# Optimization experiments

Measured on AMD Instinct MI355X. Metric: run time of the kernel, lower is better.

## Reference

```python
import jax, jax.numpy as jnp
import numpy as np

B, N = 4, 8192
D = 128
DEPTH = 4
LEAF = 32
HEADS = 4
HD = D // HEADS
SLOTS = 24
RANKS = [20, 32, 52, 82]                      # rank at encoder step j (fine -> coarse)
EXP = [RANKS[j] * (2 ** j) for j in range(DEPTH)]  # HODLR head output dims


def _rope_tables(seq_len, dim):
    inv_freq = 1.0 / (10000.0 ** (jnp.arange(0, dim, 2, dtype=jnp.float32) / dim))
    t = jnp.arange(seq_len, dtype=jnp.float32)
    freqs = t[:, None] * inv_freq[None, :]
    emb = jnp.concatenate([freqs, freqs], axis=-1)   # [S, dim]
    return jnp.cos(emb), jnp.sin(emb)


def _rotate_half(x):
    x1, x2 = jnp.split(x, 2, axis=-1)
    return jnp.concatenate([-x2, x1], axis=-1)


def _layernorm(x, g, b, eps=1e-5):
    mu = jnp.mean(x, -1, keepdims=True)
    var = jnp.mean((x - mu) ** 2, -1, keepdims=True)
    return (x - mu) * jax.lax.rsqrt(var + eps) * g + b


def _block_attn(h, qkv_w, qkv_b, pw, pb, cos, sin):
    Bc, Nc, C = h.shape
    nb = Nc // LEAF
    xb = h.reshape(Bc * nb, LEAF, C)
    qkv = (xb @ qkv_w + qkv_b).reshape(Bc * nb, LEAF, 3, HEADS, HD)
    qkv = qkv.transpose(2, 0, 3, 1, 4)               # [3, BN, H, L, hd]
    q, k, v = qkv[0], qkv[1], qkv[2]
    q = q * cos + _rotate_half(q) * sin              # full-dim RoPE (rope_dim == head_dim)
    k = k * cos + _rotate_half(k) * sin
    attn = jax.nn.softmax(jnp.einsum('bhqd,bhkd->bhqk', q, k) * (HD ** -0.5), axis=-1)
    o = jnp.einsum('bhqk,bhkd->bhqd', attn, v).transpose(0, 2, 1, 3).reshape(Bc * nb, LEAF, C)
    return (o @ pw + pb).reshape(Bc, Nc, C)


def _forward(x, cen_w, cen_b, nbr_w, nbr_b, inp_w, inp_b,
             leafp_w, leafp_b, leafh_w, leafh_b, log_scale_leaf,
             ln1_g, ln1_b, qkv_w, qkv_b, attnp_w, attnp_b,
             ln2_g, ln2_b, mlp1_w, mlp1_b, mlp2_w, mlp2_b, ds_w, ds_b,
             hu_w0, hu_b0, hv_w0, hv_b0, hu_w1, hu_b1, hv_w1, hv_b1,
             hu_w2, hu_b2, hv_w2, hv_b2, hu_w3, hu_b3, hv_w3, hv_b3):
    Bx, Nx, _ = x.shape
    # --- SymmetricNeighborEmbed (24 neighbor slots, vectorized) ---
    pos_i = x[..., 0:3]
    diag_i = x[..., 3:4]
    h_center = jnp.concatenate([pos_i, diag_i], -1) @ cen_w + cen_b          # [B,N,D]
    nb_feat = x[..., 4:4 + 5 * SLOTS].reshape(Bx, Nx, SLOTS, 5)
    rel = nb_feat[..., 0:1]
    pos_j = nb_feat[..., 1:4]
    w_ij = nb_feat[..., 4:5]
    active = (w_ij != 0.0).astype(x.dtype)
    feat = jnp.concatenate([rel * active, (pos_j - pos_i[:, :, None, :]) * active, w_ij], -1)
    e = (feat @ nbr_w + nbr_b) * active                                       # [B,N,24,D]
    h = h_center + jnp.sum(e, axis=2)
    h = h @ inp_w + inp_b
    # --- leaf dense diagonal blocks ---
    nl = Nx // LEAF
    hl = h.reshape(Bx, nl, LEAF, D) @ leafp_w + leafp_b                       # [B,nl,32,32]
    u_leaf = hl @ leafh_w + leafh_b
    dense = jnp.einsum('blik,bljk->blij', u_leaf, u_leaf) * jnp.exp(log_scale_leaf)
    diag_a = x[..., 3]                                                        # scale_A defaults to 1.0
    mask = jnp.abs(diag_a) > 1e-6
    new_diag = jnp.where(mask, 1.0 / jnp.where(mask, diag_a, 1.0), 1.0).reshape(Bx, nl, LEAF)
    dense = dense + new_diag[..., :, None] * jnp.eye(LEAF, dtype=x.dtype)
    # --- down-only encoder: transformer block -> HODLR head -> 2:1 downsample ---
    cos, sin = _rope_tables(LEAF, HD)
    hu = [(hu_w0, hu_b0), (hu_w1, hu_b1), (hu_w2, hu_b2), (hu_w3, hu_b3)]
    hv = [(hv_w0, hv_b0), (hv_w1, hv_b1), (hv_w2, hv_b2), (hv_w3, hv_b3)]
    us, vs = [], []
    for j in range(DEPTH):
        a = _block_attn(_layernorm(h, ln1_g[j], ln1_b[j]),
                        qkv_w[j], qkv_b[j], attnp_w[j], attnp_b[j], cos, sin)
        h = h + a
        m = _layernorm(h, ln2_g[j], ln2_b[j])
        m = jax.nn.gelu(m @ mlp1_w[j] + mlp1_b[j], approximate=False) @ mlp2_w[j] + mlp2_b[j]
        h = h + m
        us.append((h @ hu[j][0] + hu[j][1]).reshape(Bx, Nx, RANKS[j]))
        vs.append((h @ hv[j][0] + hv[j][1]).reshape(Bx, Nx, RANKS[j]))
        Bh, n, c = h.shape
        h = h.reshape(Bh, n // 2, 2 * c) @ ds_w[j] + ds_b[j]
    # single flat output: dense leaf blocks + all U/V HODLR factors
    return jnp.concatenate([dense.reshape(Bx, -1),
                            jnp.concatenate(us, -1).reshape(Bx, -1),
                            jnp.concatenate(vs, -1).reshape(Bx, -1)], -1)


def setup_inputs():
    key = jax.random.key(0)
    ks = iter(jax.random.split(key, 64))
    def rn(shape, s=0.05):
        return jax.random.normal(next(ks), shape, jnp.float32) * s
    z = lambda *s: jnp.zeros(s, jnp.float32)
    o = lambda *s: jnp.ones(s, jnp.float32)
    inp = {
        'x': jax.random.normal(next(ks), (B, N, 4 + 5 * SLOTS), jnp.float32),
        'cen_w': rn((4, D)), 'cen_b': z(D),
        'nbr_w': rn((5, D)), 'nbr_b': z(D),
        'inp_w': rn((D, D)), 'inp_b': z(D),
        'leafp_w': rn((D, LEAF)), 'leafp_b': z(LEAF),
        'leafh_w': rn((LEAF, LEAF), 0.01), 'leafh_b': z(LEAF),
        'log_scale_leaf': jnp.full((1,), np.log(0.01), jnp.float32),
        'ln1_g': o(DEPTH, D), 'ln1_b': z(DEPTH, D),
        'qkv_w': rn((DEPTH, D, 3 * D)), 'qkv_b': z(DEPTH, 3 * D),
        'attnp_w': rn((DEPTH, D, D)), 'attnp_b': z(DEPTH, D),
        'ln2_g': o(DEPTH, D), 'ln2_b': z(DEPTH, D),
        'mlp1_w': rn((DEPTH, D, 4 * D)), 'mlp1_b': z(DEPTH, 4 * D),
        'mlp2_w': rn((DEPTH, 4 * D, D)), 'mlp2_b': z(DEPTH, D),
        'ds_w': rn((DEPTH, 2 * D, D)), 'ds_b': z(DEPTH, D),
    }
    for j in range(DEPTH):
        inp['hu_w%d' % j] = rn((D, EXP[j]), 0.01)
        inp['hu_b%d' % j] = z(EXP[j])
        inp['hv_w%d' % j] = rn((D, EXP[j]), 0.01)
        inp['hv_b%d' % j] = z(EXP[j])
    return inp


def reference(x, cen_w, cen_b, nbr_w, nbr_b, inp_w, inp_b,
              leafp_w, leafp_b, leafh_w, leafh_b, log_scale_leaf,
              ln1_g, ln1_b, qkv_w, qkv_b, attnp_w, attnp_b,
              ln2_g, ln2_b, mlp1_w, mlp1_b, mlp2_w, mlp2_b, ds_w, ds_b,
              hu_w0, hu_b0, hv_w0, hv_b0, hu_w1, hu_b1, hv_w1, hv_b1,
              hu_w2, hu_b2, hv_w2, hv_b2, hu_w3, hu_b3, hv_w3, hv_b3):
    return _forward(x, cen_w, cen_b, nbr_w, nbr_b, inp_w, inp_b,
                    leafp_w, leafp_b, leafh_w, leafh_b, log_scale_leaf,
                    ln1_g, ln1_b, qkv_w, qkv_b, attnp_w, attnp_b,
                    ln2_g, ln2_b, mlp1_w, mlp1_b, mlp2_w, mlp2_b, ds_w, ds_b,
                    hu_w0, hu_b0, hv_w0, hv_b0, hu_w1, hu_b1, hv_w1, hv_b1,
                    hu_w2, hu_b2, hv_w2, hv_b2, hu_w3, hu_b3, hv_w3, hv_b3)
```

## Files before the change

kernel.cpp:

```cpp
#include <hip/hip_runtime.h>
#include <math.h>

#define DEV __device__ __forceinline__

constexpr int XFv = 124;
constexpr size_t OPB   = 3309568;
constexpr size_t UBASE = 262144;
constexpr size_t VBASE = 1785856;
constexpr int UVWID = 186;

using bfrag  = __attribute__((ext_vector_type(8))) short;
using f32x4v = __attribute__((ext_vector_type(4))) float;

DEV float* at4p(float* base, int t, int c0, int W) {
  return base + t * W + ((c0 + 4 * t) & (W - 1));
}
DEV float& at1r(float* base, int t, int c, int W) {
  return base[t * W + (((c & ~3) + 4 * t) & (W - 1)) + (c & 3)];
}
DEV float4 ld4g(const float* p) { return *(const float4*)p; }
DEV void fma4(float4& a, float s, const float4& w) {
  a.x += s * w.x; a.y += s * w.y; a.z += s * w.z; a.w += s * w.w;
}
DEV float gelu_fast(float x) {
  float x2 = x * x;
  float z = x * (1.5957691216057308f + 0.0713551f * x2);
  float e = __expf(z);
  float r = 1.0f - __frcp_rn(e + 1.0f);
  return x * r;
}
DEV ushort f2bf(float x) {
  unsigned u = __float_as_uint(x);
  unsigned r = (u + 0x7fffu + ((u >> 16) & 1u)) >> 16;
  return (ushort)r;
}
DEV void stb128(ushort* b, int row, int col, float v) {
  b[row * 128 + (((col & ~7) + 8 * row) & 127) + (col & 7)] = f2bf(v);
}

__global__ __launch_bounds__(256) void wprep_all_kernel(
    const float* __restrict__ src0, ushort* __restrict__ dst0, int K, int N) {
  size_t off = (size_t)blockIdx.z * K * N;
  const float* src = src0 + off;
  ushort* dst = dst0 + off;
  __shared__ float S[64][65];
  int tid = threadIdx.x;
  int k0 = blockIdx.x * 64, n0 = blockIdx.y * 64;
  for (int i = tid; i < 64 * 64; i += 256) {
    int kk = i >> 6, nn = i & 63;
    S[kk][nn] = src[(size_t)(k0 + kk) * N + n0 + nn];
  }
  __syncthreads();
  int n = tid >> 2, kq = tid & 3;
  unsigned pk[8];
#pragma unroll
  for (int i = 0; i < 8; i++) {
    int k = kq * 16 + 2 * i;
    pk[i] = (unsigned)f2bf(S[k][n]) | ((unsigned)f2bf(S[k + 1][n]) << 16);
  }
  unsigned* dp = (unsigned*)&dst[(size_t)(n0 + n) * K + k0 + kq * 16];
#pragma unroll
  for (int i = 0; i < 8; i++) dp[i] = pk[i];
}

struct UVDesc {
  const float* src[8];
  ushort* dst[8];
  int expj[8];
  int npad[8];
};
__global__ __launch_bounds__(256) void uvprep_all_kernel(UVDesc d) {
  int mi = blockIdx.y;
  int i = blockIdx.x * 256 + threadIdx.x;
  int expj = d.expj[mi];
  if (i >= d.npad[mi] * 128) return;
  int n = i >> 7, k = i & 127;
  d.dst[mi][(size_t)n * 128 + k] =
      (n < expj) ? f2bf(d.src[mi][(size_t)k * expj + n]) : (ushort)0;
}

__global__ __launch_bounds__(128) void weff_prep_kernel(
    const float* __restrict__ cw, const float* __restrict__ cb,
    const float* __restrict__ nw, const float* __restrict__ nb,
    const float* __restrict__ iw, const float* __restrict__ ib,
    float* __restrict__ weff, float* __restrict__ ropetab) {
  __shared__ float S[11 * 128];
  int tid = threadIdx.x;
  for (int i = tid; i < 512; i += 128) S[i] = cw[i];
  for (int i = tid; i < 640; i += 128) S[512 + i] = nw[i];
  S[1152 + tid] = nb[tid];
  S[1280 + tid] = cb[tid];
  __syncthreads();
  float acc[11];
#pragma unroll
  for (int r = 0; r < 10; r++) acc[r] = 0.f;
  acc[10] = ib[tid];
  for (int k = 0; k < 128; k++) {
    float w = iw[k * 128 + tid];
#pragma unroll
    for (int r = 0; r < 11; r++) acc[r] += S[r * 128 + k] * w;
  }
#pragma unroll
  for (int r = 0; r < 11; r++) weff[r * 128 + tid] = acc[r];
  for (int idx = tid; idx < 512; idx += 128) {
    int pos = idx >> 4, d = idx & 15;
    float ang = (float)pos * expf(-0.57564627324851148f * (float)d);
    ropetab[idx] = cosf(ang);
    ropetab[512 + idx] = sinf(ang);
  }
}

__global__ __launch_bounds__(256) void node_embed2_kernel(
    const float* __restrict__ x, const float* __restrict__ weff,
    float* __restrict__ h) {
  __shared__ float XR[64 * XFv];
  __shared__ float RF[64][11];
  __shared__ __align__(16) float WE[11 * 128];
  int tid = threadIdx.x;
  int node0 = blockIdx.x * 64;
  for (int i = tid; i < 64 * XFv; i += 256)
    XR[i] = x[(size_t)node0 * XFv + i];
  for (int i = tid; i < 11 * 128; i += 256) WE[i] = weff[i];
  __syncthreads();
  {
    int nn = tid >> 2, sl = tid & 3;
    const float* xr = XR + nn * XFv;
    float p0 = xr[0], p1 = xr[1], p2 = xr[2];
    float g[6] = {0.f, 0.f, 0.f, 0.f, 0.f, 0.f};
#pragma unroll
    for (int s = 0; s < 6; s++) {
      const float* f = xr + 4 + 5 * (sl * 6 + s);
      float w = f[4];
      if (w != 0.0f) {
        g[0] += f[0]; g[1] += f[1] - p0; g[2] += f[2] - p1;
        g[3] += f[3] - p2; g[4] += w; g[5] += 1.0f;
      }
    }
#pragma unroll
    for (int i = 0; i < 6; i++) {
      g[i] += __shfl_xor(g[i], 1);
      g[i] += __shfl_xor(g[i], 2);
    }
    if (sl == 0) {
      RF[nn][0] = p0; RF[nn][1] = p1; RF[nn][2] = p2; RF[nn][3] = xr[3];
#pragma unroll
      for (int i = 0; i < 6; i++) RF[nn][4 + i] = g[i];
    }
  }
  __syncthreads();
  {
    int w = tid >> 6, lane = tid & 63;
    int c4 = lane & 31, hi = lane >> 5;
    const float4* WE4 = (const float4*)WE;
#pragma unroll
    for (int rr = 0; rr < 8; rr++) {
      int node = w * 16 + rr * 2 + hi;
      float4 acc = WE4[10 * 32 + c4];
#pragma unroll
      for (int f = 0; f < 10; f++)
        fma4(acc, RF[node][f], WE4[f * 32 + c4]);
      *(float4*)&h[(size_t)(node0 + node) * 128 + c4 * 4] = acc;
    }
  }
}

__global__ __launch_bounds__(256) void leaf_dense_kernel(
    const float* __restrict__ h, const float* __restrict__ x,
    const float* __restrict__ lpw, const float* __restrict__ lpb,
    const float* __restrict__ lhw, const float* __restrict__ lhb,
    const float* __restrict__ lsc, float* __restrict__ out) {
  __shared__ __align__(16) float HS[32 * 128];
  __shared__ __align__(16) float HL[32 * 32];
  __shared__ __align__(16) float UL[32 * 32];
  int tid = threadIdx.x;
  int leaf = blockIdx.x;
  size_t base = (size_t)leaf * (32 * 128);
  for (int i = tid; i < 32 * 128; i += 256) {
    int t = i >> 7, c = i & 127;
    at1r(HS, t, c, 128) = h[base + i];
  }
  __syncthreads();
  int t = tid & 31, cg = tid >> 5;
  {
    float4 acc = ld4g(&lpb[4 * cg]);
    for (int k4 = 0; k4 < 128; k4 += 4) {
      float4 xv = *(const float4*)at4p(HS, t, k4, 128);
      float xa[4] = {xv.x, xv.y, xv.z, xv.w};
#pragma unroll
      for (int kk = 0; kk < 4; kk++)
        fma4(acc, xa[kk], ld4g(&lpw[(k4 + kk) * 32 + 4 * cg]));
    }
    *(float4*)at4p(HL, t, 4 * cg, 32) = acc;
  }
  __syncthreads();
  {
    float4 acc = ld4g(&lhb[4 * cg]);
    for (int k4 = 0; k4 < 32; k4 += 4) {
      float4 xv = *(const float4*)at4p(HL, t, k4, 32);
      float xa[4] = {xv.x, xv.y, xv.z, xv.w};
#pragma unroll
      for (int kk = 0; kk < 4; kk++)
        fma4(acc, xa[kk], ld4g(&lhw[(k4 + kk) * 32 + 4 * cg]));
    }
    *(float4*)at4p(UL, t, 4 * cg, 32) = acc;
  }
  __syncthreads();
  {
    float scale = expf(lsc[0]);
    float acc[4] = {0.f, 0.f, 0.f, 0.f};
    for (int k4 = 0; k4 < 32; k4 += 4) {
      float4 xv = *(const float4*)at4p(UL, t, k4, 32);
      float xa[4] = {xv.x, xv.y, xv.z, xv.w};
#pragma unroll
      for (int kk = 0; kk < 4; kk++) {
        int k = k4 + kk;
#pragma unroll
        for (int i2 = 0; i2 < 4; i2++)
          acc[i2] += xa[kk] * at1r(UL, 4 * cg + i2, k, 32);
      }
    }
    int b = leaf >> 8, l = leaf & 255;
#pragma unroll
    for (int i2 = 0; i2 < 4; i2++) {
      int c = 4 * cg + i2;
      float v = acc[i2] * scale;
      if (c == t) {
        float dg = x[(size_t)(leaf * 32 + t) * XFv + 3];
        v += (fabsf(dg) > 1e-6f) ? (1.0f / dg) : 1.0f;
      }
      out[(size_t)b * OPB + (size_t)l * 1024 + t * 32 + c] = v;
    }
  }
}

__global__ __launch_bounds__(256, 4) void layer_mfma_kernel(
    float* __restrict__ h,
    const float* __restrict__ lng, const float* __restrict__ lnb,
    const ushort* __restrict__ wqkvt, const float* __restrict__ bqkv,
    const ushort* __restrict__ wpt, const float* __restrict__ pb,
    const float* __restrict__ rt,
    const float* __restrict__ ln2g, const float* __restrict__ ln2b,
    const ushort* __restrict__ w1t, const float* __restrict__ b1,
    const ushort* __restrict__ w2t, const float* __restrict__ b2) {
  __shared__ __align__(16) ushort SM[20480];
  ushort* XN = SM;
  ushort* QB = SM + 4096;
  ushort* KB = SM + 8192;
  ushort* VT = SM + 12288;
  ushort* HC1 = SM + 16384;
  float*  HS = (float*)(SM + 8192);
  int tid = threadIdx.x;
  size_t base = (size_t)blockIdx.x * (32 * 128);
  int w = tid >> 6, l = tid & 63, lm = l & 15, q = l >> 4;

  {
    int m8 = tid >> 3, p8 = tid & 7;
    const float* row = h + base + m8 * 128 + p8 * 16;
    float v[16];
    float s = 0.f;
#pragma unroll
    for (int i = 0; i < 16; i += 4) {
      float4 t4 = ld4g(row + i);
      v[i] = t4.x; v[i + 1] = t4.y; v[i + 2] = t4.z; v[i + 3] = t4.w;
      s += t4.x + t4.y + t4.z + t4.w;
    }
    s += __shfl_xor(s, 1); s += __shfl_xor(s, 2); s += __shfl_xor(s, 4);
    float mu = s * (1.0f / 128.0f);
    float s2 = 0.f;
#pragma unroll
    for (int i = 0; i < 16; i++) { float d = v[i] - mu; s2 += d * d; }
    s2 += __shfl_xor(s2, 1); s2 += __shfl_xor(s2, 2); s2 += __shfl_xor(s2, 4);
    float rs = rsqrtf(s2 * (1.0f / 128.0f) + 1e-5f);
    unsigned* XW = (unsigned*)XN;
#pragma unroll
    for (int i = 0; i < 16; i += 2) {
      int c = p8 * 16 + i;
      float x0 = (v[i] - mu) * rs * lng[c] + lnb[c];
      float x1 = (v[i + 1] - mu) * rs * lng[c + 1] + lnb[c + 1];
      int kp = c >> 1;
      XW[m8 * 64 + ((kp + 4 * m8) & 63)] =
          (unsigned)f2bf(x0) | ((unsigned)f2bf(x1) << 16);
    }
  }
  __syncthreads();

  {
    f32x4v acc[2][6];
#pragma unroll
    for (int mt = 0; mt < 2; mt++)
#pragma unroll
      for (int nt = 0; nt < 6; nt++) acc[mt][nt] = (f32x4v){0.f, 0.f, 0.f, 0.f};
    for (int ks = 0; ks < 4; ks++) {
      bfrag a[2];
#pragma unroll
      for (int mt = 0; mt < 2; mt++) {
        int mm = mt * 16 + lm;
        a[mt] = *(const bfrag*)&XN[mm * 128 + ((ks * 32 + q * 8 + 8 * mm) & 127)];
      }
#pragma unroll
      for (int nt = 0; nt < 6; nt++) {
        int n = w * 96 + nt * 16 + lm;
        bfrag b = *(const bfrag*)&wqkvt[(size_t)n * 128 + ks * 32 + q * 8];
#pragma unroll
        for (int mt = 0; mt < 2; mt++)
          acc[mt][nt] = __builtin_amdgcn_mfma_f32_16x16x32_bf16(
              a[mt], b, acc[mt][nt], 0, 0, 0);
      }
    }
    float csA[4] = {}, snA[4] = {}, csB[4] = {}, snB[4] = {};
    if (w < 3) {
#pragma unroll
      for (int r = 0; r < 4; r++) {
        int pa = q * 4 + r;
        csA[r] = rt[pa * 16 + lm];        snA[r] = rt[512 + pa * 16 + lm];
        csB[r] = rt[(pa + 16) * 16 + lm]; snB[r] = rt[512 + (pa + 16) * 16 + lm];
      }
    }
#pragma unroll
    for (int p2 = 0; p2 < 3; p2++) {
      int g = w * 6 + 2 * p2;
      int ne = g * 16 + lm;
      if (g < 16) {
        float be = bqkv[ne], bo = bqkv[ne + 16];
        ushort* dst = (g < 8) ? QB : KB;
        int de = (g < 8) ? ne : ne - 128;
#pragma unroll
        for (int mt = 0; mt < 2; mt++)
#pragma unroll
          for (int r = 0; r < 4; r++) {
            int mm = mt * 16 + q * 4 + r;
            float cs = (mt & 1) ? csB[r] : csA[r];
            float sn = (mt & 1) ? snB[r] : snA[r];
            float e = acc[mt][2 * p2][r] + be;
            float o = acc[mt][2 * p2 + 1][r] + bo;
            stb128(dst, mm, de, e * cs - o * sn);
            stb128(dst, mm, de + 16, o * cs + e * sn);
          }
      } else {
#pragma unroll
        for (int h2 = 0; h2 < 2; h2++) {
          int nt = 2 * p2 + h2;
          int nv = (g + h2) * 16 + lm;
          int dv = nv - 256;
          float bv = bqkv[nv];
#pragma unroll
          for (int mt = 0; mt < 2; mt++) {
            int t0 = mt * 16 + q * 4;
            short4 pk;
            pk.x = (short)f2bf(acc[mt][nt][0] + bv);
            pk.y = (short)f2bf(acc[mt][nt][1] + bv);
            pk.z = (short)f2bf(acc[mt][nt][2] + bv);
            pk.w = (short)f2bf(acc[mt][nt][3] + bv);
            *(short4*)&VT[dv * 32 + (((t0 & ~7) + 8 * dv) & 31) + (t0 & 7)] = pk;
          }
        }
      }
    }
  }
  __syncthreads();

  ushort* SP = XN;
  {
    int head = w;
    f32x4v sc[2][2];
#pragma unroll
    for (int a2 = 0; a2 < 2; a2++)
#pragma unroll
      for (int b2 = 0; b2 < 2; b2++) sc[a2][b2] = (f32x4v){0.f, 0.f, 0.f, 0.f};
    bfrag qa[2], kb[2];
#pragma unroll
    for (int mt2 = 0; mt2 < 2; mt2++) {
      int row = mt2 * 16 + lm;
      qa[mt2] = *(const bfrag*)&QB[row * 128 + ((head * 32 + q * 8 + 8 * row) & 127)];
    }
#pragma unroll
    for (int nt2 = 0; nt2 < 2; nt2++) {
      int kt = nt2 * 16 + lm;
      kb[nt2] = *(const bfrag*)&KB[kt * 128 + ((head * 32 + q * 8 + 8 * kt) & 127)];
    }
#pragma unroll
    for (int mt2 = 0; mt2 < 2; mt2++)
#pragma unroll
      for (int nt2 = 0; nt2 < 2; nt2++)
        sc[mt2][nt2] = __builtin_amdgcn_mfma_f32_16x16x32_bf16(
            qa[mt2], kb[nt2], sc[mt2][nt2], 0, 0, 0);
    const float scl = 0.17677669529663688f;
#pragma unroll
    for (int mt2 = 0; mt2 < 2; mt2++)
#pragma unroll
      for (int nt2 = 0; nt2 < 2; nt2++)
#pragma unroll
        for (int r = 0; r < 4; r++) {
          int qt = mt2 * 16 + q * 4 + r;
          int kc = nt2 * 16 + lm;
          SP[head * 1024 + qt * 32 + (((kc & ~7) + 8 * qt) & 31) + (kc & 7)] =
              f2bf(sc[mt2][nt2][r] * scl);
        }
  }
  __syncthreads();

  {
    int rowid = tid >> 1, half = tid & 1;
    int head = rowid >> 5, qt = rowid & 31;
    ushort* rowp = SP + head * 1024 + qt * 32 + half * 16;
    float v[16];
#pragma unroll
    for (int pc = 0; pc < 2; pc++) {
      uint4 ch = *(const uint4*)&rowp[pc * 8];
      unsigned uu[4] = {ch.x, ch.y, ch.z, ch.w};
#pragma unroll
      for (int i2 = 0; i2 < 4; i2++) {
        v[pc * 8 + 2 * i2]     = __uint_as_float(uu[i2] << 16);
        v[pc * 8 + 2 * i2 + 1] = __uint_as_float(uu[i2] & 0xffff0000u);
      }
    }
    float mx = -1e30f;
#pragma unroll
    for (int i = 0; i < 16; i++) mx = fmaxf(mx, v[i]);
    mx = fmaxf(mx, __shfl_xor(mx, 1));
    float s = 0.f;
#pragma unroll
    for (int i = 0; i < 16; i++) { v[i] = __expf(v[i] - mx); s += v[i]; }
    s += __shfl_xor(s, 1);
    float inv = 1.0f / s;
#pragma unroll
    for (int pc = 0; pc < 2; pc++) {
      uint4 ch;
      unsigned uu[4];
#pragma unroll
      for (int i2 = 0; i2 < 4; i2++)
        uu[i2] = (unsigned)f2bf(v[pc * 8 + 2 * i2] * inv) |
                 ((unsigned)f2bf(v[pc * 8 + 2 * i2 + 1] * inv) << 16);
      ch.x = uu[0]; ch.y = uu[1]; ch.z = uu[2]; ch.w = uu[3];
      *(uint4*)&rowp[pc * 8] = ch;
    }
  }
  __syncthreads();

  ushort* OB = QB;
  {
    int head = w;
    f32x4v ov[2][2];
#pragma unroll
    for (int a2 = 0; a2 < 2; a2++)
#pragma unroll
      for (int b2 = 0; b2 < 2; b2++) ov[a2][b2] = (f32x4v){0.f, 0.f, 0.f, 0.f};
    bfrag pa[2], vb2[2];
#pragma unroll
    for (int mt2 = 0; mt2 < 2; mt2++) {
      int qt = mt2 * 16 + lm;
      pa[mt2] = *(const bfrag*)&SP[head * 1024 + qt * 32 + ((q * 8 + 8 * qt) & 31)];
    }
#pragma unroll
    for (int nt2 = 0; nt2 < 2; nt2++) {
      int gdim = head * 32 + nt2 * 16 + lm;
      vb2[nt2] = *(const bfrag*)&VT[gdim * 32 + ((q * 8 + 8 * gdim) & 31)];
    }
#pragma unroll
    for (int mt2 = 0; mt2 < 2; mt2++)
#pragma unroll
      for (int nt2 = 0; nt2 < 2; nt2++)
        ov[mt2][nt2] = __builtin_amdgcn_mfma_f32_16x16x32_bf16(
            pa[mt2], vb2[nt2], ov[mt2][nt2], 0, 0, 0);
#pragma unroll
    for (int mt2 = 0; mt2 < 2; mt2++)
#pragma unroll
      for (int nt2 = 0; nt2 < 2; nt2++)
#pragma unroll
        for (int r = 0; r < 4; r++) {
          int qt = mt2 * 16 + q * 4 + r;
          int gdim = head * 32 + nt2 * 16 + lm;
          stb128(OB, qt, gdim, ov[mt2][nt2][r]);
        }
  }
  __syncthreads();

  {
    f32x4v po[2][2];
#pragma unroll
    for (int mt = 0; mt < 2; mt++)
#pragma unroll
      for (int nt = 0; nt < 2; nt++) po[mt][nt] = (f32x4v){0.f, 0.f, 0.f, 0.f};
    for (int ks = 0; ks < 4; ks++) {
      bfrag a[2];
#pragma unroll
      for (int mt = 0; mt < 2; mt++) {
        int mm = mt * 16 + lm;
        a[mt] = *(const bfrag*)&OB[mm * 128 + ((ks * 32 + q * 8 + 8 * mm) & 127)];
      }
#pragma unroll
      for (int nt = 0; nt < 2; nt++) {
        int n = w * 32 + nt * 16 + lm;
        bfrag b = *(const bfrag*)&wpt[(size_t)n * 128 + ks * 32 + q * 8];
#pragma unroll
        for (int mt = 0; mt < 2; mt++)
          po[mt][nt] = __builtin_amdgcn_mfma_f32_16x16x32_bf16(
              a[mt], b, po[mt][nt], 0, 0, 0);
      }
    }
#pragma unroll
    for (int nt = 0; nt < 2; nt++) {
      int n = w * 32 + nt * 16 + lm;
      float bv = pb[n];
#pragma unroll
      for (int mt = 0; mt < 2; mt++)
#pragma unroll
        for (int r = 0; r < 4; r++) {
          int mm = mt * 16 + q * 4 + r;
          at1r(HS, mm, n, 128) = po[mt][nt][r] + bv;
        }
    }
  }
  __syncthreads();

  {
    int j = tid & 31;
    int c0 = j * 4;
    float g0 = ln2g[c0], g1 = ln2g[c0 + 1], g2 = ln2g[c0 + 2], g3 = ln2g[c0 + 3];
    float e0 = ln2b[c0], e1 = ln2b[c0 + 1], e2 = ln2b[c0 + 2], e3 = ln2b[c0 + 3];
    unsigned* XW = (unsigned*)XN;
#pragma unroll
    for (int k2 = 0; k2 < 4; k2++) {
      int idx = tid + 256 * k2;
      int tok = idx >> 5;
      float4 hg = ld4g(&h[base + (size_t)idx * 4]);
      float4 ao = *(const float4*)at4p(HS, tok, 4 * j, 128);
      float4 hn;
      hn.x = hg.x + ao.x; hn.y = hg.y + ao.y;
      hn.z = hg.z + ao.z; hn.w = hg.w + ao.w;
      *(float4*)at4p(HS, tok, 4 * j, 128) = hn;
      float s = hn.x + hn.y + hn.z + hn.w;
      s += __shfl_xor(s, 1); s += __shfl_xor(s, 2); s += __shfl_xor(s, 4);
      s += __shfl_xor(s, 8); s += __shfl_xor(s, 16);
      float mu = s * (1.0f / 128.0f);
      float d0 = hn.x - mu, d1 = hn.y - mu, d2 = hn.z - mu, d3 = hn.w - mu;
      float s2 = d0 * d0 + d1 * d1 + d2 * d2 + d3 * d3;
      s2 += __shfl_xor(s2, 1); s2 += __shfl_xor(s2, 2); s2 += __shfl_xor(s2, 4);
      s2 += __shfl_xor(s2, 8); s2 += __shfl_xor(s2, 16);
      float rs = rsqrtf(s2 * (1.0f / 128.0f) + 1e-5f);
      float x0 = d0 * rs * g0 + e0;
      float x1 = d1 * rs * g1 + e1;
      float x2 = d2 * rs * g2 + e2;
      float x3 = d3 * rs * g3 + e3;
      int kp = 2 * j;
      XW[tok * 64 + ((kp + 4 * tok) & 63)] =
          (unsigned)f2bf(x0) | ((unsigned)f2bf(x1) << 16);
      XW[tok * 64 + ((kp + 1 + 4 * tok) & 63)] =
          (unsigned)f2bf(x2) | ((unsigned)f2bf(x3) << 16);
    }
  }
  __syncthreads();

  ushort* HC0 = QB;
  f32x4v acc2[2][2];
#pragma unroll
  for (int mt = 0; mt < 2; mt++)
#pragma unroll
    for (int nt = 0; nt < 2; nt++) acc2[mt][nt] = (f32x4v){0.f, 0.f, 0.f, 0.f};

  auto mlp1_calc = [&](int hc, f32x4v A1[2][2]) {
#pragma unroll
    for (int mt = 0; mt < 2; mt++)
#pragma unroll
      for (int nt = 0; nt < 2; nt++) A1[mt][nt] = (f32x4v){0.f, 0.f, 0.f, 0.f};
#pragma unroll
    for (int ks = 0; ks < 4; ks++) {
      bfrag a[2];
#pragma unroll
      for (int mt = 0; mt < 2; mt++) {
        int mm = mt * 16 + lm;
        a[mt] = *(const bfrag*)&XN[mm * 128 + ((ks * 32 + q * 8 + 8 * mm) & 127)];
      }
#pragma unroll
      for (int nt = 0; nt < 2; nt++) {
        int n = hc * 128 + w * 32 + nt * 16 + lm;
        bfrag b = *(const bfrag*)&w1t[(size_t)n * 128 + ks * 32 + q * 8];
#pragma unroll
        for (int mt = 0; mt < 2; mt++)
          A1[mt][nt] = __builtin_amdgcn_mfma_f32_16x16x32_bf16(
              a[mt], b, A1[mt][nt], 0, 0, 0);
      }
    }
  };
  auto gelu_store = [&](int hc, f32x4v A1[2][2], ushort* HCd) {
#pragma unroll
    for (int nt = 0; nt < 2; nt++) {
      int nl = w * 32 + nt * 16 + lm;
      float b1v = b1[hc * 128 + nl];
#pragma unroll
      for (int mt = 0; mt < 2; mt++)
#pragma unroll
        for (int r = 0; r < 4; r++) {
          int mm = mt * 16 + q * 4 + r;
          float val = gelu_fast(A1[mt][nt][r] + b1v);
          HCd[mm * 128 + (((nl & ~7) + 8 * mm) & 127) + (nl & 7)] = f2bf(val);
        }
    }
  };
  auto mlp2_calc = [&](int hc, ushort* HCr) {
#pragma unroll
    for (int ks = 0; ks < 4; ks++) {
      bfrag a[2];
#pragma unroll
      for (int mt = 0; mt < 2; mt++) {
        int mm = mt * 16 + lm;
        a[mt] = *(const bfrag*)&HCr[mm * 128 + ((ks * 32 + q * 8 + 8 * mm) & 127)];
      }
#pragma unroll
      for (int nt = 0; nt < 2; nt++) {
        int n = w * 32 + nt * 16 + lm;
        bfrag b = *(const bfrag*)&w2t[(size_t)n * 512 + hc * 128 + ks * 32 + q * 8];
#pragma unroll
        for (int mt = 0; mt < 2; mt++)
          acc2[mt][nt] = __builtin_amdgcn_mfma_f32_16x16x32_bf16(
              a[mt], b, acc2[mt][nt], 0, 0, 0);
      }
    }
  };

  f32x4v a1A[2][2], a1B[2][2];
  mlp1_calc(0, a1A);
  gelu_store(0, a1A, HC0);
  __syncthreads();
  mlp1_calc(1, a1B);
  mlp2_calc(0, HC0);
  gelu_store(1, a1B, HC1);
  __syncthreads();
  mlp1_calc(2, a1A);
  mlp2_calc(1, HC1);
  gelu_store(2, a1A, HC0);
  __syncthreads();
  mlp1_calc(3, a1B);
  mlp2_calc(2, HC0);
  gelu_store(3, a1B, HC1);
  __syncthreads();
  mlp2_calc(3, HC1);

#pragma unroll
  for (int nt = 0; nt < 2; nt++) {
    int n = w * 32 + nt * 16 + lm;
    float b2v = b2[n];
#pragma unroll
    for (int mt = 0; mt < 2; mt++)
#pragma unroll
      for (int r = 0; r < 4; r++) {
        int mm = mt * 16 + q * 4 + r;
        h[base + (size_t)mm * 128 + n] = at1r(HS, mm, n, 128) + acc2[mt][nt][r] + b2v;
      }
  }
}

template <int EXPJ, int RANK, int LVL, int NSPLIT>
__global__ __launch_bounds__(256) void uvds_kernel(
    const float* __restrict__ h,
    const ushort* __restrict__ uwt, const float* __restrict__ ub,
    const ushort* __restrict__ vwt, const float* __restrict__ vb,
    float* __restrict__ ustg, float* __restrict__ vstg,
    float* __restrict__ hout,
    const ushort* __restrict__ dwt, const float* __restrict__ dsb) {
  constexpr int NT16 = (EXPJ + 15) / 16;
  constexpr int NJOBS = 2 * NT16;
  __shared__ __align__(16) ushort XN[64 * 128];
  int tid = threadIdx.x;
  int t0 = blockIdx.x * 64;
  size_t base = (size_t)t0 * 128;
  {
    int m = tid >> 2, p = tid & 3;
    const float* row = h + base + m * 128 + p * 32;
    unsigned* XW = (unsigned*)XN;
#pragma unroll
    for (int i = 0; i < 32; i += 4) {
      float4 t4 = ld4g(row + i);
      int kp = (p * 32 + i) >> 1;
      XW[m * 64 + ((kp + 4 * m) & 63)] =
          (unsigned)f2bf(t4.x) | ((unsigned)f2bf(t4.y) << 16);
      XW[m * 64 + ((kp + 1 + 4 * m) & 63)] =
          (unsigned)f2bf(t4.z) | ((unsigned)f2bf(t4.w) << 16);
    }
  }
  __syncthreads();
  int w = tid >> 6, l = tid & 63, lm = l & 15, q = l >> 4;
  int gw = w + 4 * blockIdx.y;
  for (int jj = gw; jj < NJOBS; jj += 4 * NSPLIT) {
    int uvsel = jj & 1, nt = jj >> 1;
    const ushort* wt = uvsel ? vwt : uwt;
    const float* bias = uvsel ? vb : ub;
    float* stg = uvsel ? vstg : ustg;
    f32x4v acc[4];
#pragma unroll
    for (int mt = 0; mt < 4; mt++) acc[mt] = (f32x4v){0.f, 0.f, 0.f, 0.f};
    for (int ks = 0; ks < 4; ks++) {
      bfrag b = *(const bfrag*)&wt[(size_t)(nt * 16 + lm) * 128 + ks * 32 + q * 8];
#pragma unroll
      for (int mt = 0; mt < 4; mt++) {
        int mm = mt * 16 + lm;
        int ke = ks * 32 + q * 8;
        bfrag a = *(const bfrag*)&XN[mm * 128 + ((ke + 8 * mm) & 127)];
        acc[mt] = __builtin_amdgcn_mfma_f32_16x16x32_bf16(a, b, acc[mt], 0, 0, 0);
      }
    }
    int c = nt * 16 + lm;
    if (c < EXPJ) {
      float bv = bias[c];
#pragma unroll
      for (int mt = 0; mt < 4; mt++)
#pragma unroll
        for (int r = 0; r < 4; r++) {
          int mm = mt * 16 + q * 4 + r;
          stg[(size_t)(t0 + mm) * EXPJ + c] = acc[mt][r] + bv;
        }
    }
  }
  if constexpr (LVL < 3) {
    if (blockIdx.y == 0) {
      f32x4v dacc[2][2];
#pragma unroll
      for (int mt = 0; mt < 2; mt++)
#pragma unroll
        for (int nt = 0; nt < 2; nt++) dacc[mt][nt] = (f32x4v){0.f, 0.f, 0.f, 0.f};
      for (int ks = 0; ks < 8; ks++) {
        bfrag a[2];
#pragma unroll
        for (int mt = 0; mt < 2; mt++) {
          int rr = mt * 16 + lm;
          int tok = 2 * rr + (ks >> 2);
          int c2 = (ks & 3) * 32 + q * 8;
          a[mt] = *(const bfrag*)&XN[tok * 128 + ((c2 + 8 * tok) & 127)];
        }
#pragma unroll
        for (int nt = 0; nt < 2; nt++) {
          int n = w * 32 + nt * 16 + lm;
          bfrag b = *(const bfrag*)&dwt[(size_t)n * 256 + ks * 32 + q * 8];
#pragma unroll
          for (int mt = 0; mt < 2; mt++)
            dacc[mt][nt] = __builtin_amdgcn_mfma_f32_16x16x32_bf16(
                a[mt], b, dacc[mt][nt], 0, 0, 0);
        }
      }
      size_t ob2 = (size_t)blockIdx.x * (32 * 128);
#pragma unroll
      for (int nt = 0; nt < 2; nt++) {
        int n = w * 32 + nt * 16 + lm;
        float bv = dsb[n];
#pragma unroll
        for (int mt = 0; mt < 2; mt++)
#pragma unroll
          for (int r = 0; r < 4; r++) {
            int mm = mt * 16 + q * 4 + r;
            hout[ob2 + (size_t)mm * 128 + n] = dacc[mt][nt][r] + bv;
          }
      }
    }
  }
}

struct StgPtrs { const float* u[4]; const float* v[4]; };
__global__ __launch_bounds__(256) void uv_assemble_kernel(
    StgPtrs sp, float* __restrict__ out) {
  __shared__ unsigned char JL[93];
  __shared__ unsigned char CM[93];
  int tid = threadIdx.x;
  if (tid < 93) {
    int c = 2 * tid;
    int j = (c < 20) ? 0 : (c < 52) ? 1 : (c < 104) ? 2 : 3;
    int coff = (j == 0) ? 0 : (j == 1) ? 20 : (j == 2) ? 52 : 104;
    JL[tid] = (unsigned char)j;
    CM[tid] = (unsigned char)(c - coff);
  }
  __syncthreads();
  int g0 = blockIdx.x * 32;
  for (int i = tid; i < 32 * 93; i += 256) {
    int rr = i / 93, cp = i - rr * 93;
    int g = g0 + rr;
    int b = g >> 13, n = g & 8191;
    int j = JL[cp], cm = CM[cp];
    int expj, rank;
    if (j == 0)      { expj = 20;  rank = 20; }
    else if (j == 1) { expj = 64;  rank = 32; }
    else if (j == 2) { expj = 208; rank = 52; }
    else             { expj = 656; rank = 82; }
    int tok = (b << (13 - j)) + (n >> j);
    int cdiv = n & ((1 << j) - 1);
    size_t si = (size_t)tok * expj + cdiv * rank + cm;
    size_t ob = (size_t)b * OPB + (size_t)n * UVWID + 2 * cp;
    *(float2*)&out[ob + UBASE] = *(const float2*)&sp.u[j][si];
    *(float2*)&out[ob + VBASE] = *(const float2*)&sp.v[j][si];
  }
}

extern "C" void kernel_launch(void* const* d_in, const int* in_sizes, int n_in,
                              void* d_out, int out_size, void* d_ws, size_t ws_size,
                              hipStream_t stream) {
  const float* x       = (const float*)d_in[0];
  const float* cen_w   = (const float*)d_in[1];
  const float* cen_b   = (const float*)d_in[2];
  const float* nbr_w   = (const float*)d_in[3];
  const float* nbr_b   = (const float*)d_in[4];
  const float* inp_w   = (const float*)d_in[5];
  const float* inp_b   = (const float*)d_in[6];
  const float* leafp_w = (const float*)d_in[7];
  const float* leafp_b = (const float*)d_in[8];
  const float* leafh_w = (const float*)d_in[9];
  const float* leafh_b = (const float*)d_in[10];
  const float* lscale  = (const float*)d_in[11];
  const float* ln1_g   = (const float*)d_in[12];
  const float* ln1_b   = (const float*)d_in[13];
  const float* qkv_w   = (const float*)d_in[14];
  const float* qkv_b   = (const float*)d_in[15];
  const float* attnp_w = (const float*)d_in[16];
  const float* attnp_b = (const float*)d_in[17];
  const float* ln2_g   = (const float*)d_in[18];
  const float* ln2_b   = (const float*)d_in[19];
  const float* mlp1_w  = (const float*)d_in[20];
  const float* mlp1_b  = (const float*)d_in[21];
  const float* mlp2_w  = (const float*)d_in[22];
  const float* mlp2_b  = (const float*)d_in[23];
  const float* ds_w    = (const float*)d_in[24];
  const float* ds_b    = (const float*)d_in[25];
  const float* huw[4], *hub[4], *hvw[4], *hvb[4];
  for (int j = 0; j < 4; j++) {
    huw[j] = (const float*)d_in[26 + 4 * j];
    hub[j] = (const float*)d_in[27 + 4 * j];
    hvw[j] = (const float*)d_in[28 + 4 * j];
    hvb[j] = (const float*)d_in[29 + 4 * j];
  }
  float* out = (float*)d_out;
  float* hA = (float*)d_ws;
  float* hB = hA + (size_t)4 * 8192 * 128;
  ushort* w1t = (ushort*)(hB + (size_t)2097152);
  ushort* w2t = w1t + (size_t)4 * 65536;
  ushort* uvt = w2t + (size_t)4 * 65536;
  const int NPAD[4] = {32, 64, 208, 656};
  ushort* uwt[4]; ushort* vwt[4];
  ushort* p = uvt;
  for (int j = 0; j < 4; j++) {
    uwt[j] = p; p += (size_t)NPAD[j] * 128;
    vwt[j] = p; p += (size_t)NPAD[j] * 128;
  }
  ushort* wqkvt = p;
  ushort* wpt   = wqkvt + (size_t)4 * 384 * 128;
  ushort* dswt  = wpt + (size_t)4 * 128 * 128;
  float* weff   = (float*)(dswt + (size_t)4 * 128 * 256);
  float* ropetab = weff + 1408;
  const size_t STG[4] = {32768ull * 20, 16384ull * 64, 8192ull * 208, 4096ull * 656};
  float* ustg[4]; float* vstg[4];
  float* sp2 = ropetab + 1024;
  for (int j = 0; j < 4; j++) {
    ustg[j] = sp2; sp2 += STG[j];
    vstg[j] = sp2; sp2 += STG[j];
  }
  const int EXPJ_[4] = {20, 64, 208, 656};

  weff_prep_kernel<<<1, 128, 0, stream>>>(
      cen_w, cen_b, nbr_w, nbr_b, inp_w, inp_b, weff, ropetab);
  wprep_all_kernel<<<dim3(2, 8, 4), 256, 0, stream>>>(mlp1_w, w1t, 128, 512);
  wprep_all_kernel<<<dim3(8, 2, 4), 256, 0, stream>>>(mlp2_w, w2t, 512, 128);
  wprep_all_kernel<<<dim3(2, 6, 4), 256, 0, stream>>>(qkv_w, wqkvt, 128, 384);
  wprep_all_kernel<<<dim3(2, 2, 4), 256, 0, stream>>>(attnp_w, wpt, 128, 128);
  wprep_all_kernel<<<dim3(4, 2, 4), 256, 0, stream>>>(ds_w, dswt, 256, 128);
  {
    UVDesc d;
    for (int j = 0; j < 4; j++) {
      d.src[2 * j] = huw[j];     d.dst[2 * j] = uwt[j];
      d.src[2 * j + 1] = hvw[j]; d.dst[2 * j + 1] = vwt[j];
      d.expj[2 * j] = EXPJ_[j];  d.expj[2 * j + 1] = EXPJ_[j];
      d.npad[2 * j] = NPAD[j];   d.npad[2 * j + 1] = NPAD[j];
    }
    uvprep_all_kernel<<<dim3(328, 8), 256, 0, stream>>>(d);
  }

  node_embed2_kernel<<<(4 * 8192) / 64, 256, 0, stream>>>(x, weff, hA);
  leaf_dense_kernel<<<(4 * 8192) / 32, 256, 0, stream>>>(
      hA, x, leafp_w, leafp_b, leafh_w, leafh_b, lscale, out);

  layer_mfma_kernel<<<32768 / 32, 256, 0, stream>>>(
      hA, ln1_g, ln1_b, wqkvt, qkv_b, wpt, attnp_b, ropetab,
      ln2_g, ln2_b, w1t, mlp1_b, w2t, mlp2_b);
  uvds_kernel<20, 20, 0, 1><<<dim3(512, 1), 256, 0, stream>>>(
      hA, uwt[0], hub[0], vwt[0], hvb[0], ustg[0], vstg[0],
      hB, dswt, ds_b);

  layer_mfma_kernel<<<16384 / 32, 256, 0, stream>>>(
      hB, ln1_g + 128, ln1_b + 128, wqkvt + 49152, qkv_b + 384,
      wpt + 16384, attnp_b + 128, ropetab,
      ln2_g + 128, ln2_b + 128, w1t + 65536, mlp1_b + 512,
      w2t + 65536, mlp2_b + 128);
  uvds_kernel<64, 32, 1, 2><<<dim3(256, 2), 256, 0, stream>>>(
      hB, uwt[1], hub[1], vwt[1], hvb[1], ustg[1], vstg[1],
      hA, dswt + 32768, ds_b + 128);

  layer_mfma_kernel<<<8192 / 32, 256, 0, stream>>>(
      hA, ln1_g + 256, ln1_b + 256, wqkvt + 98304, qkv_b + 768,
      wpt + 32768, attnp_b + 256, ropetab,
      ln2_g + 256, ln2_b + 256, w1t + 131072, mlp1_b + 1024,
      w2t + 131072, mlp2_b + 256);
  uvds_kernel<208, 52, 2, 4><<<dim3(128, 4), 256, 0, stream>>>(
      hA, uwt[2], hub[2], vwt[2], hvb[2], ustg[2], vstg[2],
      hB, dswt + 65536, ds_b + 256);

  layer_mfma_kernel<<<4096 / 32, 256, 0, stream>>>(
      hB, ln1_g + 384, ln1_b + 384, wqkvt + 147456, qkv_b + 1152,
      wpt + 49152, attnp_b + 384, ropetab,
      ln2_g + 384, ln2_b + 384, w1t + 196608, mlp1_b + 1536,
      w2t + 196608, mlp2_b + 384);
  uvds_kernel<656, 82, 3, 8><<<dim3(64, 8), 256, 0, stream>>>(
      hB, uwt[3], hub[3], vwt[3], hvb[3], ustg[3], vstg[3],
      hA , dswt , ds_b );

  {
    StgPtrs sp;
    for (int j = 0; j < 4; j++) { sp.u[j] = ustg[j]; sp.v[j] = vstg[j]; }
    uv_assemble_kernel<<<32768 / 32, 256, 0, stream>>>(sp, out);
  }
  (void)in_sizes; (void)n_in; (void)out_size; (void)ws_size;
}
```

Measured before the change: 419.7 us.

## Fuse HODLR U/V heads and downsample into transformer layer epilogue

For the first three levels, the layer kernel now keeps its final residual output in shared memory, converts it to bf16, and computes the U/V head projections and the 2:1 downsample GEMM directly in its epilogue. This removes the separate uvds launches and the global round trip of the layer output for those levels. The last level still uses the standalone uvds kernel without the downsample. The cost is that all U/V output tiles for a 32-token block are now handled by only four waves, which serializes more work per block and adds shared-memory pressure and syncs to the layer kernel.

```diff
diff --git a/kernel.cpp b/kernel.cpp
--- a/kernel.cpp
+++ b/kernel.cpp
@@ -233,6 +233,7 @@
   }
 }
 
+template <int EXPJ, int RANK, int LVL, bool FUSE>
 __global__ __launch_bounds__(256, 4) void layer_mfma_kernel(
     float* __restrict__ h,
     const float* __restrict__ lng, const float* __restrict__ lnb,
@@ -241,7 +242,12 @@
     const float* __restrict__ rt,
     const float* __restrict__ ln2g, const float* __restrict__ ln2b,
     const ushort* __restrict__ w1t, const float* __restrict__ b1,
-    const ushort* __restrict__ w2t, const float* __restrict__ b2) {
+    const ushort* __restrict__ w2t, const float* __restrict__ b2,
+    const ushort* __restrict__ uwt, const float* __restrict__ ub,
+    const ushort* __restrict__ vwt, const float* __restrict__ vb,
+    float* __restrict__ ustg, float* __restrict__ vstg,
+    float* __restrict__ hout,
+    const ushort* __restrict__ dwt, const float* __restrict__ dsb) {
   __shared__ __align__(16) ushort SM[20480];
   ushort* XN = SM;
   ushort* QB = SM + 4096;
@@ -636,17 +642,114 @@
   __syncthreads();
   mlp2_calc(3, HC1);
 
-#pragma unroll
-  for (int nt = 0; nt < 2; nt++) {
-    int n = w * 32 + nt * 16 + lm;
-    float b2v = b2[n];
-#pragma unroll
-    for (int mt = 0; mt < 2; mt++)
-#pragma unroll
-      for (int r = 0; r < 4; r++) {
-        int mm = mt * 16 + q * 4 + r;
-        h[base + (size_t)mm * 128 + n] = at1r(HS, mm, n, 128) + acc2[mt][nt][r] + b2v;
-      }
+  if constexpr (!FUSE) {
+#pragma unroll
+    for (int nt = 0; nt < 2; nt++) {
+      int n = w * 32 + nt * 16 + lm;
+      float b2v = b2[n];
+#pragma unroll
+      for (int mt = 0; mt < 2; mt++)
+#pragma unroll
+        for (int r = 0; r < 4; r++) {
+          int mm = mt * 16 + q * 4 + r;
+          h[base + (size_t)mm * 128 + n] = at1r(HS, mm, n, 128) + acc2[mt][nt][r] + b2v;
+        }
+    }
+  } else {
+#pragma unroll
+    for (int nt = 0; nt < 2; nt++) {
+      int n = w * 32 + nt * 16 + lm;
+      float b2v = b2[n];
+#pragma unroll
+      for (int mt = 0; mt < 2; mt++)
+#pragma unroll
+        for (int r = 0; r < 4; r++) {
+          int mm = mt * 16 + q * 4 + r;
+          at1r(HS, mm, n, 128) += acc2[mt][nt][r] + b2v;
+        }
+    }
+    __syncthreads();
+
+    {
+      int j = tid & 31;
+      unsigned* XW = (unsigned*)XN;
+#pragma unroll
+      for (int k2 = 0; k2 < 4; k2++) {
+        int idx = tid + 256 * k2;
+        int tok = idx >> 5;
+        float4 hv = *(const float4*)at4p(HS, tok, 4 * j, 128);
+        int kp = 2 * j;
+        XW[tok * 64 + ((kp + 4 * tok) & 63)] =
+            (unsigned)f2bf(hv.x) | ((unsigned)f2bf(hv.y) << 16);
+        XW[tok * 64 + ((kp + 1 + 4 * tok) & 63)] =
+            (unsigned)f2bf(hv.z) | ((unsigned)f2bf(hv.w) << 16);
+      }
+    }
+    __syncthreads();
+
+    {
+      constexpr int NT16 = (EXPJ + 15) / 16;
+      constexpr int NJOBS = 2 * NT16;
+      int t0 = blockIdx.x * 32;
+      for (int jj = w; jj < NJOBS; jj += 4) {
+        int uvsel = jj & 1, nt = jj >> 1;
+        const ushort* wt = uvsel ? vwt : uwt;
+        const float* bias = uvsel ? vb : ub;
+        float* stg = uvsel ? vstg : ustg;
+        f32x4v acc[2];
+        acc[0] = (f32x4v){0.f, 0.f, 0.f, 0.f};
+        acc[1] = (f32x4v){0.f, 0.f, 0.f, 0.f};
+        for (int ks = 0; ks < 4; ks++) {
+          bfrag b = *(const bfrag*)&wt[(size_t)(nt * 16 + lm) * 128 + ks * 32 + q * 8];
+#pragma unroll
+          for (int mt = 0; mt < 2; mt++) {
+            int mm = mt * 16 + lm;
+            int ke = ks * 32 + q * 8;
+            bfrag a = *(const bfrag*)&XN[mm * 128 + ((ke + 8 * mm) & 127)];
+            acc[mt] = __builtin_amdgcn_mfma_f32_16x16x32_bf16(a, b, acc[mt], 0, 0, 0);
+          }
+        }
+        int c = nt * 16 + lm;
+        if (c < EXPJ) {
+          float bv = bias[c];
+#pragma unroll
+          for (int mt = 0; mt < 2; mt++)
+#pragma unroll
+            for (int r = 0; r < 4; r++) {
+              int mm = mt * 16 + q * 4 + r;
+              stg[(size_t)(t0 + mm) * EXPJ + c] = acc[mt][r] + bv;
+            }
+        }
+      }
+    }
+
+    {
+      f32x4v dacc[2];
+      dacc[0] = (f32x4v){0.f, 0.f, 0.f, 0.f};
+      dacc[1] = (f32x4v){0.f, 0.f, 0.f, 0.f};
+      for (int ks = 0; ks < 8; ks++) {
+        int mm = 2 * lm + (ks >> 2);
+        int col = (ks & 3) * 32 + q * 8;
+        bfrag a = *(const bfrag*)&XN[mm * 128 + ((col + 8 * mm) & 127)];
+#pragma unroll
+        for (int nt = 0; nt < 2; nt++) {
+          int n = w * 32 + nt * 16 + lm;
+          bfrag b = *(const bfrag*)&dwt[(size_t)n * 256 + ks * 32 + q * 8];
+          dacc[nt] = __builtin_amdgcn_mfma_f32_16x16x32_bf16(a, b, dacc[nt], 0, 0, 0);
+        }
+      }
+      size_t obase2 = (size_t)blockIdx.x * (16 * 128);
+#pragma unroll
+      for (int nt = 0; nt < 2; nt++) {
+        int n = w * 32 + nt * 16 + lm;
+        float bv = dsb[n];
+#pragma unroll
+        for (int r = 0; r < 4; r++) {
+          int mm = q * 4 + r;
+          hout[obase2 + (size_t)mm * 128 + n] = dacc[nt][r] + bv;
+        }
+      }
+    }
   }
 }
 
@@ -655,9 +758,7 @@
     const float* __restrict__ h,
     const ushort* __restrict__ uwt, const float* __restrict__ ub,
     const ushort* __restrict__ vwt, const float* __restrict__ vb,
-    float* __restrict__ ustg, float* __restrict__ vstg,
-    float* __restrict__ hout,
-    const ushort* __restrict__ dwt, const float* __restrict__ dsb) {
+    float* __restrict__ ustg, float* __restrict__ vstg) {
   constexpr int NT16 = (EXPJ + 15) / 16;
   constexpr int NJOBS = 2 * NT16;
   __shared__ __align__(16) ushort XN[64 * 128];
@@ -709,47 +810,6 @@
           int mm = mt * 16 + q * 4 + r;
           stg[(size_t)(t0 + mm) * EXPJ + c] = acc[mt][r] + bv;
         }
-    }
-  }
-  if constexpr (LVL < 3) {
-    if (blockIdx.y == 0) {
-      f32x4v dacc[2][2];
-#pragma unroll
-      for (int mt = 0; mt < 2; mt++)
-#pragma unroll
-        for (int nt = 0; nt < 2; nt++) dacc[mt][nt] = (f32x4v){0.f, 0.f, 0.f, 0.f};
-      for (int ks = 0; ks < 8; ks++) {
-        bfrag a[2];
-#pragma unroll
-        for (int mt = 0; mt < 2; mt++) {
-          int rr = mt * 16 + lm;
-          int tok = 2 * rr + (ks >> 2);
-          int c2 = (ks & 3) * 32 + q * 8;
-          a[mt] = *(const bfrag*)&XN[tok * 128 + ((c2 + 8 * tok) & 127)];
-        }
-#pragma unroll
-        for (int nt = 0; nt < 2; nt++) {
-          int n = w * 32 + nt * 16 + lm;
-          bfrag b = *(const bfrag*)&dwt[(size_t)n * 256 + ks * 32 + q * 8];
-#pragma unroll
-          for (int mt = 0; mt < 2; mt++)
-            dacc[mt][nt] = __builtin_amdgcn_mfma_f32_16x16x32_bf16(
-                a[mt], b, dacc[mt][nt], 0, 0, 0);
-        }
-      }
-      size_t ob2 = (size_t)blockIdx.x * (32 * 128);
-#pragma unroll
-      for (int nt = 0; nt < 2; nt++) {
-        int n = w * 32 + nt * 16 + lm;
-        float bv = dsb[n];
-#pragma unroll
-        for (int mt = 0; mt < 2; mt++)
-#pragma unroll
-          for (int r = 0; r < 4; r++) {
-            int mm = mt * 16 + q * 4 + r;
-            hout[ob2 + (size_t)mm * 128 + n] = dacc[mt][nt][r] + bv;
-          }
-      }
     }
   }
 }
@@ -873,39 +933,37 @@
   leaf_dense_kernel<<<(4 * 8192) / 32, 256, 0, stream>>>(
       hA, x, leafp_w, leafp_b, leafh_w, leafh_b, lscale, out);
 
-  layer_mfma_kernel<<<32768 / 32, 256, 0, stream>>>(
+  layer_mfma_kernel<20, 20, 0, true><<<32768 / 32, 256, 0, stream>>>(
       hA, ln1_g, ln1_b, wqkvt, qkv_b, wpt, attnp_b, ropetab,
-      ln2_g, ln2_b, w1t, mlp1_b, w2t, mlp2_b);
-  uvds_kernel<20, 20, 0, 1><<<dim3(512, 1), 256, 0, stream>>>(
-      hA, uwt[0], hub[0], vwt[0], hvb[0], ustg[0], vstg[0],
+      ln2_g, ln2_b, w1t, mlp1_b, w2t, mlp2_b,
+      uwt[0], hub[0], vwt[0], hvb[0], ustg[0], vstg[0],
       hB, dswt, ds_b);
 
-  layer_mfma_kernel<<<16384 / 32, 256, 0, stream>>>(
+  layer_mfma_kernel<64, 32, 1, true><<<16384 / 32, 256, 0, stream>>>(
       hB, ln1_g + 128, ln1_b + 128, wqkvt + 49152, qkv_b + 384,
       wpt + 16384, attnp_b + 128, ropetab,
       ln2_g + 128, ln2_b + 128, w1t + 65536, mlp1_b + 512,
-      w2t + 65536, mlp2_b + 128);
-  uvds_kernel<64, 32, 1, 2><<<dim3(256, 2), 256, 0, stream>>>(
-      hB, uwt[1], hub[1], vwt[1], hvb[1], ustg[1], vstg[1],
+      w2t + 65536, mlp2_b + 128,
+      uwt[1], hub[1], vwt[1], hvb[1], ustg[1], vstg[1],
       hA, dswt + 32768, ds_b + 128);
 
-  layer_mfma_kernel<<<8192 / 32, 256, 0, stream>>>(
+  layer_mfma_kernel<208, 52, 2, true><<<8192 / 32, 256, 0, stream>>>(
       hA, ln1_g + 256, ln1_b + 256, wqkvt + 98304, qkv_b + 768,
       wpt + 32768, attnp_b + 256, ropetab,
       ln2_g + 256, ln2_b + 256, w1t + 131072, mlp1_b + 1024,
-      w2t + 131072, mlp2_b + 256);
-  uvds_kernel<208, 52, 2, 4><<<dim3(128, 4), 256, 0, stream>>>(
-      hA, uwt[2], hub[2], vwt[2], hvb[2], ustg[2], vstg[2],
+      w2t + 131072, mlp2_b + 256,
+      uwt[2], hub[2], vwt[2], hvb[2], ustg[2], vstg[2],
       hB, dswt + 65536, ds_b + 256);
 
-  layer_mfma_kernel<<<4096 / 32, 256, 0, stream>>>(
+  layer_mfma_kernel<656, 82, 3, false><<<4096 / 32, 256, 0, stream>>>(
       hB, ln1_g + 384, ln1_b + 384, wqkvt + 147456, qkv_b + 1152,
       wpt + 49152, attnp_b + 384, ropetab,
       ln2_g + 384, ln2_b + 384, w1t + 196608, mlp1_b + 1536,
-      w2t + 196608, mlp2_b + 384);
+      w2t + 196608, mlp2_b + 384,
+      uwt[3], hub[3], vwt[3], hvb[3], ustg[3], vstg[3],
+      hA , dswt , ds_b );
   uvds_kernel<656, 82, 3, 8><<<dim3(64, 8), 256, 0, stream>>>(
-      hB, uwt[3], hub[3], vwt[3], hvb[3], ustg[3], vstg[3],
-      hA , dswt , ds_b );
+      hB, uwt[3], hub[3], vwt[3], hvb[3], ustg[3], vstg[3]);
 
   {
     StgPtrs sp;
```

Result: slower. 432.8 us (+3.1%).
